# Kernel tuning notes

Hardware: AMD Instinct MI355X
Metric: run time of the kernel (lower is better)

Reference implementation:

```python
import jax, jax.numpy as jnp
import numpy as np

CROP_SIZE = (14, 14)
NUM_LEVELS = 5
CANONICAL_SIZE = 224.0
CANONICAL_LEVEL = 1.0
EPS = 1e-7  # keras.backend.epsilon()


def _map_to_level(boxes):
    # boxes: [N, 4] (x1, y1, x2, y2) in image pixels
    w = boxes[:, 2] - boxes[:, 0]
    h = boxes[:, 3] - boxes[:, 1]
    size = jnp.sqrt(w * h)
    lv = jnp.floor(CANONICAL_LEVEL + jnp.log2(size / CANONICAL_SIZE + EPS))
    return jnp.clip(lv, 0.0, NUM_LEVELS - 1.0)


def _crop_and_resize(img, boxes, crop_size):
    # TF tf.image.crop_and_resize semantics (bilinear, extrapolation_value=0).
    # img: [H, W, C]; boxes: [N, 4] normalized (y1, x1, y2, x2)
    H, W, _ = img.shape
    ch, cw = crop_size
    y1, x1, y2, x2 = boxes[:, 0], boxes[:, 1], boxes[:, 2], boxes[:, 3]
    ty = jnp.arange(ch, dtype=boxes.dtype) / (ch - 1)
    tx = jnp.arange(cw, dtype=boxes.dtype) / (cw - 1)
    ys = (y1[:, None] * (1 - ty) + y2[:, None] * ty) * (H - 1)  # [N, ch]
    xs = (x1[:, None] * (1 - tx) + x2[:, None] * tx) * (W - 1)  # [N, cw]

    def corners(c, size):
        lo = jnp.floor(c)
        frac = c - lo
        lo_i = jnp.clip(lo, 0, size - 1).astype(jnp.int32)
        hi_i = jnp.clip(lo + 1, 0, size - 1).astype(jnp.int32)
        valid = (c >= 0) & (c <= size - 1)
        return lo_i, hi_i, frac, valid

    y0, y1i, fy, vy = corners(ys, H)
    x0, x1i, fx, vx = corners(xs, W)
    # gather 4 corners: [N, ch, cw, C]
    tl = img[y0[:, :, None], x0[:, None, :]]
    tr = img[y0[:, :, None], x1i[:, None, :]]
    bl = img[y1i[:, :, None], x0[:, None, :]]
    br = img[y1i[:, :, None], x1i[:, None, :]]
    fxb = fx[:, None, :, None]
    fyb = fy[:, :, None, None]
    top = tl + (tr - tl) * fxb
    bot = bl + (br - bl) * fxb
    out = top + (bot - top) * fyb
    mask = (vy[:, :, None] & vx[:, None, :])[:, :, :, None]
    return jnp.where(mask, out, 0.0)


def _roi_align(image_shape, boxes, scores, fpn):
    img_h = image_shape[1].astype(jnp.float32)
    img_w = image_shape[2].astype(jnp.float32)
    levels = _map_to_level(boxes)
    x1b, y1b, x2b, y2b = boxes[:, 0], boxes[:, 1], boxes[:, 2], boxes[:, 3]
    out = jnp.zeros((boxes.shape[0], CROP_SIZE[0], CROP_SIZE[1], fpn[0].shape[-1]),
                    dtype=fpn[0].dtype)
    for i, f in enumerate(fpn):
        fh = jnp.float32(f.shape[0])
        fw = jnp.float32(f.shape[1])
        # exact box normalization from the keras module
        nb = jnp.stack([
            y1b / img_h * fh / (fh - 1),
            x1b / img_w * fw / (fw - 1),
            (y2b / img_h * fh - 1) / (fh - 1),
            (x2b / img_w * fw - 1) / (fw - 1)], axis=1)
        crop = _crop_and_resize(f, nb, CROP_SIZE)
        sel = (levels == i)[:, None, None, None]
        # per-box level routing (equivalent to gather -> crop -> scatter_nd)
        out = out + jnp.where(sel, crop, 0.0)
    return out[None]  # [1, N, ch, cw, C]


def setup_inputs() -> dict:
    key = jax.random.key(0)
    ks = jax.random.split(key, 10)
    N, C, IMG = 512, 256, 1024.0
    cx = jax.random.uniform(ks[0], (N,), minval=16.0, maxval=IMG - 16.0)
    cy = jax.random.uniform(ks[1], (N,), minval=16.0, maxval=IMG - 16.0)
    # log-uniform box sizes 16..512 px so all 5 FPN levels are populated
    sz = jnp.exp(jax.random.uniform(ks[2], (N,), minval=jnp.log(16.0), maxval=jnp.log(512.0)))
    ar = jnp.exp(jax.random.uniform(ks[3], (N,), minval=jnp.log(0.5), maxval=jnp.log(2.0)))
    w = sz * jnp.sqrt(ar)
    h = sz / jnp.sqrt(ar)
    x1 = jnp.clip(cx - w / 2, 0.0, IMG)
    x2 = jnp.clip(cx + w / 2, 0.0, IMG)
    y1 = jnp.clip(cy - h / 2, 0.0, IMG)
    y2 = jnp.clip(cy + h / 2, 0.0, IMG)
    boxes = jnp.stack([x1, y1, x2, y2], axis=1)[None]  # [1, N, 4]
    scores = jax.random.uniform(ks[4], (1, N), dtype=jnp.float32)
    sizes = [256, 128, 64, 32, 16]  # FPN strides 4..64 on a 1024px image
    fpn = {f"fpn{i}": jax.random.normal(ks[5 + i], (1, s, s, C), dtype=jnp.float32)
           for i, s in enumerate(sizes)}
    return {"image_shape": jnp.array([1, 1024, 1024, 3], dtype=jnp.int32),
            "boxes": boxes, "scores": scores, **fpn}


def reference(image_shape, boxes, scores, fpn0, fpn1, fpn2, fpn3, fpn4):
    b = jax.lax.stop_gradient(boxes[0])
    s = jax.lax.stop_gradient(scores[0])
    fpn = [jax.lax.stop_gradient(f[0]) for f in (fpn0, fpn1, fpn2, fpn3, fpn4)]
    return _roi_align(image_shape, b, s, fpn)
```

## Files before the change

### kernel.cpp

```cpp
#include <hip/hip_runtime.h>


#define CROP 14
#define POS (CROP * CROP)
#define C 256
#define CANON 224.0f
#define EPSF 1e-7f

typedef float vfloat4 __attribute__((ext_vector_type(4)));

__device__ __forceinline__ void store_bypass(float* p, vfloat4 v) {
    asm volatile("global_store_dwordx4 %0, %1, off sc0 sc1 nt"
                 :
                 : "v"(p), "v"(v)
                 : "memory");
}

__global__ __launch_bounds__(256) void roi_align_kernel(
    const int* __restrict__ image_shape,
    const float* __restrict__ boxes,
    const float* __restrict__ f0,
    const float* __restrict__ f1,
    const float* __restrict__ f2,
    const float* __restrict__ f3,
    const float* __restrict__ f4,
    float* __restrict__ out)
{
    const int nwg = gridDim.x;
    const int q = nwg >> 3, r = nwg & 7;
    const int xcd = blockIdx.x & 7, slot = blockIdx.x >> 3;
    const int blk = (xcd < r ? xcd * (q + 1) : r * (q + 1) + (xcd - r) * q) + slot;

    const int box      = blk / 25;
    const int blkInBox = blk % 25;
    const int wave = threadIdx.x >> 6;
    const int lane = threadIdx.x & 63;
    const int p0 = blkInBox * 8 + wave * 2;

    const float imgh = (float)image_shape[1];
    const float imgw = (float)image_shape[2];
    const float bx1 = boxes[box * 4 + 0];
    const float by1 = boxes[box * 4 + 1];
    const float bx2 = boxes[box * 4 + 2];
    const float by2 = boxes[box * 4 + 3];

    const float w  = bx2 - bx1;
    const float h  = by2 - by1;
    const float sz = sqrtf(w * h);
    float lvf = floorf(1.0f + log2f(sz / CANON + EPSF));
    lvf = fminf(fmaxf(lvf, 0.0f), 4.0f);
    const int lv = (int)lvf;

    const int   s  = 256 >> lv;
    const float fh = (float)s;
    const float fw = (float)s;

    const float ny1 = by1 / imgh * fh / (fh - 1.0f);
    const float nx1 = bx1 / imgw * fw / (fw - 1.0f);
    const float ny2 = (by2 / imgh * fh - 1.0f) / (fh - 1.0f);
    const float nx2 = (bx2 / imgw * fw - 1.0f) / (fw - 1.0f);

    const float* __restrict__ f =
        (lv == 0) ? f0 : (lv == 1) ? f1 : (lv == 2) ? f2 : (lv == 3) ? f3 : f4;
    const int cbase = lane * 4;

    #pragma unroll
    for (int k = 0; k < 2; ++k) {
        const int p = p0 + k;
        if (p >= POS) continue;
        const int py = p / CROP;
        const int px = p % CROP;
        const float ty = (float)py / (float)(CROP - 1);
        const float tx = (float)px / (float)(CROP - 1);
        const float yc = (ny1 * (1.0f - ty) + ny2 * ty) * (fh - 1.0f);
        const float xc = (nx1 * (1.0f - tx) + nx2 * tx) * (fw - 1.0f);

        const float ylo = floorf(yc);
        const float fy  = yc - ylo;
        const int y0  = (int)fminf(fmaxf(ylo,        0.0f), fh - 1.0f);
        const int y1i = (int)fminf(fmaxf(ylo + 1.0f, 0.0f), fh - 1.0f);
        const bool vy = (yc >= 0.0f) && (yc <= fh - 1.0f);

        const float xlo = floorf(xc);
        const float fx  = xc - xlo;
        const int x0  = (int)fminf(fmaxf(xlo,        0.0f), fw - 1.0f);
        const int x1i = (int)fminf(fmaxf(xlo + 1.0f, 0.0f), fw - 1.0f);
        const bool vx = (xc >= 0.0f) && (xc <= fw - 1.0f);

        vfloat4 o;
        if (vy && vx) {
            const vfloat4 tl = *(const vfloat4*)(f + ((size_t)y0  * s + x0 ) * C + cbase);
            const vfloat4 tr = *(const vfloat4*)(f + ((size_t)y0  * s + x1i) * C + cbase);
            const vfloat4 bl = *(const vfloat4*)(f + ((size_t)y1i * s + x0 ) * C + cbase);
            const vfloat4 br = *(const vfloat4*)(f + ((size_t)y1i * s + x1i) * C + cbase);
            const vfloat4 top = tl + (tr - tl) * fx;
            const vfloat4 bot = bl + (br - bl) * fx;
            o = top + (bot - top) * fy;
        } else { o = (vfloat4)0.0f; }

        store_bypass(out + ((size_t)box * POS + p) * C + cbase, o);
    }
}

extern "C" void kernel_launch(void* const* d_in, const int* in_sizes, int n_in,
                              void* d_out, int out_size, void* d_ws, size_t ws_size,
                              hipStream_t stream) {
    const int*   image_shape = (const int*)d_in[0];
    const float* boxes       = (const float*)d_in[1];
    const float* f0 = (const float*)d_in[3];
    const float* f1 = (const float*)d_in[4];
    const float* f2 = (const float*)d_in[5];
    const float* f3 = (const float*)d_in[6];
    const float* f4 = (const float*)d_in[7];
    float* out = (float*)d_out;

    const int N = in_sizes[1] / 4;

    roi_align_kernel<<<N * 25, 256, 0, stream>>>(
        image_shape, boxes, f0, f1, f2, f3, f4, out);
}
```

Baseline: 52.14 us.

## Convert ROI align to persistent waves with double-buffered corner loads

Replaces the one-block-per-8-positions grid with a fixed grid of 1024 persistent blocks. Each wave processes a contiguous range of position pairs, and the four corner loads for the next pair are issued before the current pair is interpolated and stored. Box and level parameters are recomputed only when the box changes. The aim is to hide gather latency and cut launch and per-block setup cost, at the price of more registers and a fixed grid size. It also switches the inline-asm bypass store to the nontemporal builtin.

After: 59.58 us. 1.14x slower.

```diff
diff --git a/kernel.cpp b/kernel.cpp
--- a/kernel.cpp
+++ b/kernel.cpp
@@ -2,21 +2,113 @@
 
 
 #define CROP 14
-#define POS (CROP * CROP)
+#define POS 196
+#define HALF 98
 #define C 256
 #define CANON 224.0f
 #define EPSF 1e-7f
+#define NBLK 1024
 
 typedef float vfloat4 __attribute__((ext_vector_type(4)));
 
-__device__ __forceinline__ void store_bypass(float* p, vfloat4 v) {
-    asm volatile("global_store_dwordx4 %0, %1, off sc0 sc1 nt"
-                 :
-                 : "v"(p), "v"(v)
-                 : "memory");
-}
-
-__global__ __launch_bounds__(256) void roi_align_kernel(
+struct BoxState {
+    int box;
+    const float* f;
+    int s;
+    float fh, ny1, nx1, ny2, nx2;
+};
+
+struct PosP {
+    float fx, fy;
+    bool  v;
+    const float *pTL, *pTR, *pBL, *pBR;
+};
+
+__device__ __forceinline__ void update_box(
+    BoxState& bs, int box, const float* __restrict__ boxes,
+    float imgh, float imgw,
+    const float* f0, const float* f1, const float* f2,
+    const float* f3, const float* f4)
+{
+    bs.box = box;
+    const float bx1 = boxes[box * 4 + 0];
+    const float by1 = boxes[box * 4 + 1];
+    const float bx2 = boxes[box * 4 + 2];
+    const float by2 = boxes[box * 4 + 3];
+    const float w  = bx2 - bx1;
+    const float h  = by2 - by1;
+    const float sz = sqrtf(w * h);
+    float lvf = floorf(1.0f + log2f(sz / CANON + EPSF));
+    lvf = fminf(fmaxf(lvf, 0.0f), 4.0f);
+    const int lv = (int)lvf;
+    const int s  = 256 >> lv;
+    const float fh = (float)s;
+    bs.s = s; bs.fh = fh;
+    bs.f = (lv == 0) ? f0 : (lv == 1) ? f1 : (lv == 2) ? f2 : (lv == 3) ? f3 : f4;
+    bs.ny1 = by1 / imgh * fh / (fh - 1.0f);
+    bs.nx1 = bx1 / imgw * fh / (fh - 1.0f);
+    bs.ny2 = (by2 / imgh * fh - 1.0f) / (fh - 1.0f);
+    bs.nx2 = (bx2 / imgw * fh - 1.0f) / (fh - 1.0f);
+}
+
+__device__ __forceinline__ PosP pos_params(const BoxState& bs, int p, int cbase)
+{
+    const int py = p / CROP;
+    const int px = p % CROP;
+    const float ty = (float)py / (float)(CROP - 1);
+    const float tx = (float)px / (float)(CROP - 1);
+    const float yc = (bs.ny1 * (1.0f - ty) + bs.ny2 * ty) * (bs.fh - 1.0f);
+    const float xc = (bs.nx1 * (1.0f - tx) + bs.nx2 * tx) * (bs.fh - 1.0f);
+
+    const float ylo = floorf(yc);
+    const int y0  = (int)fminf(fmaxf(ylo,        0.0f), bs.fh - 1.0f);
+    const int y1i = (int)fminf(fmaxf(ylo + 1.0f, 0.0f), bs.fh - 1.0f);
+    const bool vy = (yc >= 0.0f) && (yc <= bs.fh - 1.0f);
+
+    const float xlo = floorf(xc);
+    const int x0  = (int)fminf(fmaxf(xlo,        0.0f), bs.fh - 1.0f);
+    const int x1i = (int)fminf(fmaxf(xlo + 1.0f, 0.0f), bs.fh - 1.0f);
+    const bool vx = (xc >= 0.0f) && (xc <= bs.fh - 1.0f);
+
+    PosP r;
+    r.fx = xc - xlo;
+    r.fy = yc - ylo;
+    r.v  = vy && vx;
+    r.pTL = bs.f + ((size_t)y0  * bs.s + x0 ) * C + cbase;
+    r.pTR = bs.f + ((size_t)y0  * bs.s + x1i) * C + cbase;
+    r.pBL = bs.f + ((size_t)y1i * bs.s + x0 ) * C + cbase;
+    r.pBR = bs.f + ((size_t)y1i * bs.s + x1i) * C + cbase;
+    return r;
+}
+
+#define ISSUE(P0, P1, d0,d1,d2,d3,d4,d5,d6,d7)            \
+    if (P0.v) { d0 = *(const vfloat4*)P0.pTL;             \
+                d1 = *(const vfloat4*)P0.pTR;             \
+                d2 = *(const vfloat4*)P0.pBL;             \
+                d3 = *(const vfloat4*)P0.pBR; }           \
+    if (P1.v) { d4 = *(const vfloat4*)P1.pTL;             \
+                d5 = *(const vfloat4*)P1.pTR;             \
+                d6 = *(const vfloat4*)P1.pBL;             \
+                d7 = *(const vfloat4*)P1.pBR; }
+
+#define CONSUME(P0, P1, oo, d0,d1,d2,d3,d4,d5,d6,d7)                         \
+    {                                                                         \
+        vfloat4 r0, r1;                                                       \
+        if (P0.v) {                                                           \
+            vfloat4 top = d0 + (d1 - d0) * P0.fx;                             \
+            vfloat4 bot = d2 + (d3 - d2) * P0.fx;                             \
+            r0 = top + (bot - top) * P0.fy;                                   \
+        } else r0 = (vfloat4)0.0f;                                            \
+        if (P1.v) {                                                           \
+            vfloat4 top = d4 + (d5 - d4) * P1.fx;                             \
+            vfloat4 bot = d6 + (d7 - d6) * P1.fx;                             \
+            r1 = top + (bot - top) * P1.fy;                                   \
+        } else r1 = (vfloat4)0.0f;                                            \
+        __builtin_nontemporal_store(r0, (vfloat4*)(out + (oo)));              \
+        __builtin_nontemporal_store(r1, (vfloat4*)(out + (oo) + C));          \
+    }
+
+__global__ __launch_bounds__(256, 4) void roi_align_persist(
     const int* __restrict__ image_shape,
     const float* __restrict__ boxes,
     const float* __restrict__ f0,
@@ -24,81 +116,73 @@
     const float* __restrict__ f2,
     const float* __restrict__ f3,
     const float* __restrict__ f4,
-    float* __restrict__ out)
+    float* __restrict__ out,
+    int units, int nwaves)
 {
-    const int nwg = gridDim.x;
-    const int q = nwg >> 3, r = nwg & 7;
-    const int xcd = blockIdx.x & 7, slot = blockIdx.x >> 3;
-    const int blk = (xcd < r ? xcd * (q + 1) : r * (q + 1) + (xcd - r) * q) + slot;
-
-    const int box      = blk / 25;
-    const int blkInBox = blk % 25;
+    const int blk  = blockIdx.x;
+    const int xcd  = blk & 7, slot = blk >> 3;
+    const int sblk = xcd * (gridDim.x >> 3) + slot;
     const int wave = threadIdx.x >> 6;
     const int lane = threadIdx.x & 63;
-    const int p0 = blkInBox * 8 + wave * 2;
+    const int wgid = sblk * 4 + wave;
+
+    const int K = units / nwaves, R = units % nwaves;
+    const int start = wgid * K + (wgid < R ? wgid : R);
+    const int cnt   = K + (wgid < R ? 1 : 0);
+    if (cnt <= 0) return;
 
     const float imgh = (float)image_shape[1];
     const float imgw = (float)image_shape[2];
-    const float bx1 = boxes[box * 4 + 0];
-    const float by1 = boxes[box * 4 + 1];
-    const float bx2 = boxes[box * 4 + 2];
-    const float by2 = boxes[box * 4 + 3];
-
-    const float w  = bx2 - bx1;
-    const float h  = by2 - by1;
-    const float sz = sqrtf(w * h);
-    float lvf = floorf(1.0f + log2f(sz / CANON + EPSF));
-    lvf = fminf(fmaxf(lvf, 0.0f), 4.0f);
-    const int lv = (int)lvf;
-
-    const int   s  = 256 >> lv;
-    const float fh = (float)s;
-    const float fw = (float)s;
-
-    const float ny1 = by1 / imgh * fh / (fh - 1.0f);
-    const float nx1 = bx1 / imgw * fw / (fw - 1.0f);
-    const float ny2 = (by2 / imgh * fh - 1.0f) / (fh - 1.0f);
-    const float nx2 = (bx2 / imgw * fw - 1.0f) / (fw - 1.0f);
-
-    const float* __restrict__ f =
-        (lv == 0) ? f0 : (lv == 1) ? f1 : (lv == 2) ? f2 : (lv == 3) ? f3 : f4;
     const int cbase = lane * 4;
 
-    #pragma unroll
-    for (int k = 0; k < 2; ++k) {
-        const int p = p0 + k;
-        if (p >= POS) continue;
-        const int py = p / CROP;
-        const int px = p % CROP;
-        const float ty = (float)py / (float)(CROP - 1);
-        const float tx = (float)px / (float)(CROP - 1);
-        const float yc = (ny1 * (1.0f - ty) + ny2 * ty) * (fh - 1.0f);
-        const float xc = (nx1 * (1.0f - tx) + nx2 * tx) * (fw - 1.0f);
-
-        const float ylo = floorf(yc);
-        const float fy  = yc - ylo;
-        const int y0  = (int)fminf(fmaxf(ylo,        0.0f), fh - 1.0f);
-        const int y1i = (int)fminf(fmaxf(ylo + 1.0f, 0.0f), fh - 1.0f);
-        const bool vy = (yc >= 0.0f) && (yc <= fh - 1.0f);
-
-        const float xlo = floorf(xc);
-        const float fx  = xc - xlo;
-        const int x0  = (int)fminf(fmaxf(xlo,        0.0f), fw - 1.0f);
-        const int x1i = (int)fminf(fmaxf(xlo + 1.0f, 0.0f), fw - 1.0f);
-        const bool vx = (xc >= 0.0f) && (xc <= fw - 1.0f);
-
-        vfloat4 o;
-        if (vy && vx) {
-            const vfloat4 tl = *(const vfloat4*)(f + ((size_t)y0  * s + x0 ) * C + cbase);
-            const vfloat4 tr = *(const vfloat4*)(f + ((size_t)y0  * s + x1i) * C + cbase);
-            const vfloat4 bl = *(const vfloat4*)(f + ((size_t)y1i * s + x0 ) * C + cbase);
-            const vfloat4 br = *(const vfloat4*)(f + ((size_t)y1i * s + x1i) * C + cbase);
-            const vfloat4 top = tl + (tr - tl) * fx;
-            const vfloat4 bot = bl + (br - bl) * fx;
-            o = top + (bot - top) * fy;
-        } else { o = (vfloat4)0.0f; }
-
-        store_bypass(out + ((size_t)box * POS + p) * C + cbase, o);
+    BoxState bs; bs.box = -1;
+
+    int u   = start;
+    int end = start + cnt;
+
+    int boxA = u / HALF;
+    if (boxA != bs.box) update_box(bs, boxA, boxes, imgh, imgw, f0, f1, f2, f3, f4);
+    int ppA = (u - boxA * HALF) * 2;
+    PosP a0 = pos_params(bs, ppA,     cbase);
+    PosP a1 = pos_params(bs, ppA + 1, cbase);
+    size_t ooA = (size_t)2 * (size_t)u * C + cbase;
+    vfloat4 dA0, dA1, dA2, dA3, dA4, dA5, dA6, dA7;
+    ISSUE(a0, a1, dA0, dA1, dA2, dA3, dA4, dA5, dA6, dA7);
+
+    PosP b0, b1;
+    size_t ooB = 0;
+    vfloat4 dB0, dB1, dB2, dB3, dB4, dB5, dB6, dB7;
+
+    for (;;) {
+        const bool hasB = (u + 1 < end);
+        if (hasB) {
+            const int un = u + 1;
+            const int boxB = un / HALF;
+            if (boxB != bs.box) update_box(bs, boxB, boxes, imgh, imgw, f0, f1, f2, f3, f4);
+            const int ppB = (un - boxB * HALF) * 2;
+            b0 = pos_params(bs, ppB,     cbase);
+            b1 = pos_params(bs, ppB + 1, cbase);
+            ooB = (size_t)2 * (size_t)un * C + cbase;
+            ISSUE(b0, b1, dB0, dB1, dB2, dB3, dB4, dB5, dB6, dB7);
+        }
+        CONSUME(a0, a1, ooA, dA0, dA1, dA2, dA3, dA4, dA5, dA6, dA7);
+        ++u;
+        if (!hasB) break;
+
+        const bool hasA = (u + 1 < end);
+        if (hasA) {
+            const int un = u + 1;
+            const int boxN = un / HALF;
+            if (boxN != bs.box) update_box(bs, boxN, boxes, imgh, imgw, f0, f1, f2, f3, f4);
+            const int ppN = (un - boxN * HALF) * 2;
+            a0 = pos_params(bs, ppN,     cbase);
+            a1 = pos_params(bs, ppN + 1, cbase);
+            ooA = (size_t)2 * (size_t)un * C + cbase;
+            ISSUE(a0, a1, dA0, dA1, dA2, dA3, dA4, dA5, dA6, dA7);
+        }
+        CONSUME(b0, b1, ooB, dB0, dB1, dB2, dB3, dB4, dB5, dB6, dB7);
+        ++u;
+        if (!hasA) break;
     }
 }
 
@@ -115,7 +199,9 @@
     float* out = (float*)d_out;
 
     const int N = in_sizes[1] / 4;
-
-    roi_align_kernel<<<N * 25, 256, 0, stream>>>(
-        image_shape, boxes, f0, f1, f2, f3, f4, out);
-}
+    const int units  = N * HALF;
+    const int nwaves = NBLK * 4;
+
+    roi_align_persist<<<NBLK, 256, 0, stream>>>(
+        image_shape, boxes, f0, f1, f2, f3, f4, out, units, nwaves);
+}
```
